# Optimization experiments

Measured on AMD Instinct MI355X. Metric: run time of the kernel, lower is better.

## Reference

```python
import math
import jax, jax.numpy as jnp
import numpy as np

HIDDEN = 1024
NUM_HEADS = 16
HEAD_DIM = HIDDEN // NUM_HEADS
B, S = 4, 2048


def setup_inputs() -> dict:
    key = jax.random.key(0)
    ks = jax.random.split(key, 10)
    sc_in = 1.0 / math.sqrt(HIDDEN)
    inp = {
        "query": jax.random.normal(ks[0], (B, S, HIDDEN), jnp.float32),
        "key": jax.random.normal(ks[1], (B, S, HIDDEN), jnp.float32),
        "value": jax.random.normal(ks[2], (B, S, HIDDEN), jnp.float32),
        "mask": jax.random.randint(ks[3], (B, S), 0, 2).astype(bool),
        # NOTE: ModuleList([Linear]*num_heads) shares ONE Linear across all heads.
        "Wq": jax.random.normal(ks[4], (HIDDEN, HEAD_DIM), jnp.float32) * sc_in,
        "bq": jnp.zeros((HEAD_DIM,), jnp.float32),
        "Wk": jax.random.normal(ks[5], (HIDDEN, HEAD_DIM), jnp.float32) * sc_in,
        "bk": jnp.zeros((HEAD_DIM,), jnp.float32),
        "Wv": jax.random.normal(ks[6], (HIDDEN, HEAD_DIM), jnp.float32) * sc_in,
        "bv": jnp.zeros((HEAD_DIM,), jnp.float32),
        "Wout": jax.random.normal(ks[7], (HIDDEN, HIDDEN), jnp.float32) * sc_in,
        "bout": jnp.zeros((HIDDEN,), jnp.float32),
        "seq_mask": 0,
    }
    return inp


def _layer_norm_scores(x, eps=1e-8):
    # torch.std is unbiased (ddof=1); is_train=False => no affine
    mean = jnp.mean(x, axis=-1, keepdims=True)
    sigma = jnp.std(x, axis=-1, keepdims=True, ddof=1)
    return (x - mean) / (sigma + eps)


def reference(query, key, value, mask, Wq, bq, Wk, bk, Wv, bv, Wout, bout, seq_mask):
    # All heads share identical weights -> compute one head, tile the concat.
    q = query @ Wq + bq          # [B,S,hd]
    k = key @ Wk + bk            # [B,S,hd]
    v = value @ Wv + bv          # [B,S,hd]
    scores = jnp.einsum("bqd,bkd->bqk", q, k) / math.sqrt(HIDDEN)  # [B,S,S]
    scores = _layer_norm_scores(scores)
    m = jnp.broadcast_to(mask[:, None, :], scores.shape)  # [B,S,S]
    if seq_mask:
        tri = jnp.triu(jnp.ones(scores.shape[-2:], bool), k=1)
        m = m | tri[None]
    # original fills with -1e-32 (effectively a no-op bug) -- reproduce exactly
    scores = scores + jnp.where(m, jnp.float32(-1e-32), jnp.float32(0.0))
    attn = jax.nn.softmax(scores, axis=-1)
    head = jnp.einsum("bqk,bkd->bqd", attn, v)   # [B,S,hd]
    attention = jnp.tile(head, (1, 1, NUM_HEADS))  # concat of identical heads
    return attention @ Wout + bout
```

## Files before the change

### kernel.cpp

```cpp
#include <hip/hip_runtime.h>
#include <math.h>

#define B_  4
#define S_  2048
#define H_  1024
#define D_  64
#define ROWS (B_*S_)
#define LOG2E 1.4426950408889634f

typedef __attribute__((ext_vector_type(4))) float  floatx4;
typedef __attribute__((ext_vector_type(8))) short  short8;
typedef __attribute__((ext_vector_type(8))) __bf16 bf16x8;

#define WS_KSUM 0
#define WS_M    (WS_KSUM + B_*D_)
#define WS_A2   (WS_M + B_*D_*D_)
#define WS_C2   (WS_A2 + ROWS)
#define WS_FEND (WS_C2 + ROWS)
#define WB_QB  0
#define WB_KF  (WB_QB + ROWS*D_)
#define WB_VF  (WB_KF + ROWS*D_)
#define WB_WT  (WB_VF + ROWS*D_)
#define WB_WFF (WB_WT + 3*D_*H_)
#define NZ2    (B_*D_ + B_*D_*D_)

__device__ __forceinline__ unsigned short f2bf(float f) {
    union { float f; unsigned u; } v; v.f = f;
    unsigned r = v.u + 0x7FFFu + ((v.u >> 16) & 1u);
    return (unsigned short)(r >> 16);
}
__device__ __forceinline__ short bfc(float f) {
    __bf16 h = (__bf16)f;
    short s; __builtin_memcpy(&s, &h, 2); return s;
}
__device__ __forceinline__ float bf2f(short s) {
    union { unsigned u; float f; } v;
    v.u = ((unsigned)(unsigned short)s) << 16; return v.f;
}
__device__ __forceinline__ bf16x8 ldb(const short* p) {
    union { short8 s; bf16x8 b; } u; u.s = *(const short8*)p; return u.b;
}
#define MFMA(a,b,c) __builtin_amdgcn_mfma_f32_16x16x32_bf16(a, b, c, 0, 0, 0)
__device__ __forceinline__ void lds_fence() {
    __builtin_amdgcn_wave_barrier();
    __builtin_amdgcn_s_waitcnt(0xc07f);
    __builtin_amdgcn_wave_barrier();
}

__global__ __launch_bounds__(256) void prep(
    const float* __restrict__ Wq, const float* __restrict__ Wk,
    const float* __restrict__ Wv, const float* __restrict__ Wout,
    float* __restrict__ wsf)
{
    __shared__ float tile[64][65];
    short* wsb = (short*)(wsf + WS_FEND);
    const int bx = blockIdx.x, t = threadIdx.x;
    if (bx < 96) {
        int idx = bx * 256 + t;
        int mat = idx >> 13, rem = idx & 8191;
        int kc = rem >> 8, nt = (rem >> 6) & 3, lane = rem & 63;
        int g = lane >> 4, l15 = lane & 15;
        const float* W = (mat == 0) ? Wq : (mat == 1) ? Wk : Wv;
        short8 fr;
        #pragma unroll
        for (int j = 0; j < 8; ++j)
            fr[j] = (short)f2bf(W[(size_t)(kc*32 + g*8 + j) * D_ + nt*16 + l15]);
        *(short8*)&wsb[WB_WT + (size_t)idx * 8] = fr;
    } else if (bx < 112) {
        int n0 = (bx - 96) * 64;
        int nn = t & 63, dg = t >> 6;
        for (int dd = 0; dd < 16; ++dd) {
            int d = dg * 16 + dd;
            float s = 0.0f;
            #pragma unroll
            for (int h = 0; h < 16; ++h)
                s += Wout[(size_t)(h * 64 + d) * H_ + n0 + nn];
            tile[d][nn] = s;
        }
        __syncthreads();
        #pragma unroll
        for (int u = 0; u < 2; ++u) {
            int s = 2*t + u;
            int ctl = s >> 7, h = (s >> 6) & 1, lane = s & 63;
            int g = lane >> 4, l2 = lane & 15;
            short8 fr;
            #pragma unroll
            for (int j = 0; j < 8; ++j)
                fr[j] = (short)f2bf(tile[h*32 + g*8 + j][ctl*16 + l2]);
            *(short8*)&wsb[WB_WFF + (size_t)((((n0 >> 4) + ctl)*2 + h)*64 + lane) * 8] = fr;
        }
    } else {
        int i = (bx - 112) * 256 + t;
        if (i < NZ2) wsf[WS_KSUM + i] = 0.0f;
    }
}

__global__ __launch_bounds__(256) void qkv_mfma(
    const float* __restrict__ query, const float* __restrict__ key,
    const float* __restrict__ value,
    const float* __restrict__ bq, const float* __restrict__ bk,
    const float* __restrict__ bvp, float* __restrict__ wsf)
{
    short* wsb = (short*)(wsf + WS_FEND);
    const int mat = blockIdx.y;
    const float* X    = (mat == 0) ? query : (mat == 1) ? key : value;
    const float* bias = (mat == 0) ? bq    : (mat == 1) ? bk  : bvp;
    const short* WT3 = wsb + WB_WT + (size_t)mat * (D_ * H_);

    const int t = threadIdx.x, w = t >> 6, lane = t & 63;
    const int l15 = lane & 15, g = lane >> 4;
    const int r0 = blockIdx.x * 32;
    const int mrow0 = (w >> 1) * 16;
    const int nt0 = (w & 1) * 2;

    __shared__ short xs[32][136];
    floatx4 acc[2] = {};

    for (int step = 0; step < 8; ++step) {
        __syncthreads();
        #pragma unroll
        for (int u = 0; u < 4; ++u) {
            int row = u * 8 + (t >> 5), col = (t & 31) * 4;
            float4 xv = *(const float4*)&X[(size_t)(r0 + row) * H_ + step * 128 + col];
            short4 pk;
            pk.x = bfc(xv.x); pk.y = bfc(xv.y); pk.z = bfc(xv.z); pk.w = bfc(xv.w);
            *(short4*)&xs[row][col] = pk;
        }
        __syncthreads();
        #pragma unroll
        for (int kk = 0; kk < 4; ++kk) {
            bf16x8 a = ldb(&xs[mrow0 + l15][kk * 32 + g * 8]);
            int kc = step * 4 + kk;
            #pragma unroll
            for (int n = 0; n < 2; ++n) {
                bf16x8 bf = ldb(&WT3[(size_t)((kc * 4) + nt0 + n) * 512 + lane * 8]);
                acc[n] = MFMA(a, bf, acc[n]);
            }
        }
    }

    if (mat == 0) {
        short* QB = wsb + WB_QB;
        #pragma unroll
        for (int n = 0; n < 2; ++n) {
            int col = (nt0 + n) * 16 + l15;
            float bb = bias[col];
            #pragma unroll
            for (int r = 0; r < 4; ++r)
                QB[(size_t)(r0 + mrow0 + 4*g + r) * D_ + col] = (short)f2bf(acc[n][r] + bb);
        }
    } else if (mat == 1) {
        short* KF = wsb + WB_KF;
        #pragma unroll
        for (int n = 0; n < 2; ++n) {
            int d = (nt0 + n) * 16 + l15;
            int kh = d >> 5, gk = (d >> 3) & 3, j = d & 7;
            float bb = bias[d];
            #pragma unroll
            for (int r = 0; r < 4; ++r) {
                int R = r0 + mrow0 + 4*g + r;
                KF[(size_t)(((R >> 4) * 2 + kh) * 64 + gk * 16 + (R & 15)) * 8 + j] =
                    (short)f2bf(acc[n][r] + bb);
            }
        }
    } else {
        short* VF = wsb + WB_VF;
        int R0 = r0 + mrow0 + 4*g;
        int kh = (R0 >> 5) & 1, gv = (R0 >> 3) & 3, j0 = R0 & 7, blk = R0 >> 6;
        #pragma unroll
        for (int n = 0; n < 2; ++n) {
            int d = (nt0 + n) * 16 + l15;
            int ntv = d >> 4;
            float bb = bias[d];
            short4 pk;
            pk.x = (short)f2bf(acc[n][0] + bb); pk.y = (short)f2bf(acc[n][1] + bb);
            pk.z = (short)f2bf(acc[n][2] + bb); pk.w = (short)f2bf(acc[n][3] + bb);
            *(short4*)&VF[(size_t)(((blk * 4 + ntv) * 2 + kh) * 64 + gv * 16 + (d & 15)) * 8 + j0] = pk;
        }
    }
}

__global__ __launch_bounds__(256) void kstats(float* __restrict__ wsf) {
    const short* KF = (short*)(wsf + WS_FEND) + WB_KF;
    const int b     = blockIdx.x >> 5;
    const int chunk = blockIdx.x & 31;
    const int keyblk0 = b * 128 + chunk * 4;

    __shared__ float kt[64][64];
    const int t = threadIdx.x;
    #pragma unroll
    for (int u = 0; u < 2; ++u) {
        int s = 2*t + u;
        int kb4 = s >> 7, kh = (s >> 6) & 1, lane2 = s & 63;
        int g2 = lane2 >> 4, l2 = lane2 & 15;
        short8 v = *(const short8*)&KF[(size_t)(((keyblk0 + kb4) * 2 + kh) * 64 + lane2) * 8];
        #pragma unroll
        for (int j = 0; j < 8; ++j)
            kt[kb4 * 16 + l2][kh * 32 + g2 * 8 + j] = bf2f(v[j]);
    }
    __syncthreads();

    const int td = t >> 4, te = t & 15;
    float acc[4][4] = {};
    for (int j = 0; j < 64; ++j) {
        float4 a  = *(const float4*)&kt[j][td*4];
        float4 bb = *(const float4*)&kt[j][te*4];
        float av[4] = {a.x, a.y, a.z, a.w};
        float bw[4] = {bb.x, bb.y, bb.z, bb.w};
        #pragma unroll
        for (int i = 0; i < 4; ++i)
            #pragma unroll
            for (int l = 0; l < 4; ++l)
                acc[i][l] += av[i] * bw[l];
    }
    float* M = wsf + WS_M + (size_t)b * D_ * D_;
    #pragma unroll
    for (int i = 0; i < 4; ++i)
        #pragma unroll
        for (int l = 0; l < 4; ++l)
            atomicAdd(&M[(td*4 + i) * D_ + te*4 + l], acc[i][l]);

    if (t < 64) {
        float s = 0.0f;
        for (int j = 0; j < 64; ++j) s += kt[j][t];
        atomicAdd(&wsf[WS_KSUM + b * D_ + t], s);
    }
}

__global__ __launch_bounds__(256) void rowstats(float* __restrict__ wsf) {
    const short* Qb = (short*)(wsf + WS_FEND) + WB_QB;
    const int t = threadIdx.x, w = t >> 6, lane = t & 63;
    const int q0 = blockIdx.x * 32 + w * 8;
    const int b  = q0 >> 11;
    const float* M = wsf + WS_M + (size_t)b * D_ * D_;

    float qv[8], y[8] = {};
    #pragma unroll
    for (int r = 0; r < 8; ++r) qv[r] = bf2f(Qb[(size_t)(q0 + r) * D_ + lane]);
    for (int d2 = 0; d2 < 64; ++d2) {
        float m = M[d2 * D_ + lane];
        #pragma unroll
        for (int r = 0; r < 8; ++r) y[r] += __shfl(qv[r], d2, 64) * m;
    }
    float kl = wsf[WS_KSUM + b * D_ + lane];
    float z[8], sv[8];
    #pragma unroll
    for (int r = 0; r < 8; ++r) { z[r] = y[r] * qv[r]; sv[r] = qv[r] * kl; }
    #pragma unroll
    for (int m = 1; m < 64; m <<= 1) {
        #pragma unroll
        for (int r = 0; r < 8; ++r) {
            z[r]  += __shfl_xor(z[r],  m, 64);
            sv[r] += __shfl_xor(sv[r], m, 64);
        }
    }
    #pragma unroll
    for (int r = 0; r < 8; ++r) {
        if (lane == r) {
            float sum   = sv[r] * (1.0f / 32.0f);
            float sumsq = z[r]  * (1.0f / 1024.0f);
            float mu  = sum * (1.0f / 2048.0f);
            float var = (sumsq - sum * sum * (1.0f / 2048.0f)) * (1.0f / 2047.0f);
            var = fmaxf(var, 0.0f);
            float inv = 1.0f / (sqrtf(var) + 1e-8f);
            wsf[WS_A2 + q0 + r] = inv * (LOG2E / 32.0f);
            wsf[WS_C2 + q0 + r] = -mu * inv * LOG2E;
        }
    }
}

__global__ __launch_bounds__(512, 4) void attn_fused(
    const float* __restrict__ bout, float* __restrict__ wsf,
    float* __restrict__ out)
{
    short* wsb = (short*)(wsf + WS_FEND);
    const short* Qb  = wsb + WB_QB;
    const short* KF  = wsb + WB_KF;
    const short* VF  = wsb + WB_VF;
    const short* WFF = wsb + WB_WFF;

    __shared__ short P[8][16][72];
    __shared__ short OL[8][16][64];
    __shared__ float sumwL[8][16];
    __shared__ short hnF[2 * 64 * 8];

    const int t = threadIdx.x, w = t >> 6, lane = t & 63;
    const int l15 = lane & 15, g = lane >> 4;
    const int q0 = blockIdx.x * 16;
    const int b  = blockIdx.x >> 7;

    bf16x8 bqf0 = ldb(&Qb[(size_t)(q0 + l15) * D_ + 0*32 + g*8]);
    bf16x8 bqf1 = ldb(&Qb[(size_t)(q0 + l15) * D_ + 1*32 + g*8]);
    const float a2v = wsf[WS_A2 + q0 + l15];
    const float c2v = wsf[WS_C2 + q0 + l15];

    floatx4 O[4] = {};
    float sacc = 0.0f;
    short* Pw = &P[w][0][0];

    for (int kc = 0; kc < 256; kc += 64) {
        const int key0 = w * 256 + kc;
        const int kblk16 = (b * S_ + key0) >> 4;
        const int kblk64 = (b * S_ + key0) >> 6;
        floatx4 Sc[4] = {};
        __builtin_amdgcn_s_setprio(1);
        #pragma unroll
        for (int kt = 0; kt < 4; ++kt) {
            bf16x8 ak0 = ldb(&KF[(size_t)(((kblk16 + kt) * 2 + 0) * 64 + lane) * 8]);
            bf16x8 ak1 = ldb(&KF[(size_t)(((kblk16 + kt) * 2 + 1) * 64 + lane) * 8]);
            Sc[kt] = MFMA(ak0, bqf0, Sc[kt]);
            Sc[kt] = MFMA(ak1, bqf1, Sc[kt]);
        }
        __builtin_amdgcn_s_setprio(0);
        lds_fence();
        #pragma unroll
        for (int kt = 0; kt < 4; ++kt) {
            float w0 = __builtin_amdgcn_exp2f(fmaf(Sc[kt][0], a2v, c2v));
            float w1 = __builtin_amdgcn_exp2f(fmaf(Sc[kt][1], a2v, c2v));
            float w2 = __builtin_amdgcn_exp2f(fmaf(Sc[kt][2], a2v, c2v));
            float w3 = __builtin_amdgcn_exp2f(fmaf(Sc[kt][3], a2v, c2v));
            sacc += (w0 + w1) + (w2 + w3);
            short4 pk;
            pk.x = bfc(w0); pk.y = bfc(w1); pk.z = bfc(w2); pk.w = bfc(w3);
            *(short4*)&Pw[l15 * 72 + kt*16 + 4*g] = pk;
        }
        lds_fence();
        bf16x8 ap0 = ldb(&Pw[l15 * 72 + 0*32 + g*8]);
        bf16x8 ap1 = ldb(&Pw[l15 * 72 + 1*32 + g*8]);
        __builtin_amdgcn_s_setprio(1);
        #pragma unroll
        for (int nt = 0; nt < 4; ++nt) {
            bf16x8 bv0 = ldb(&VF[(size_t)(((kblk64 * 4 + nt) * 2 + 0) * 64 + lane) * 8]);
            bf16x8 bv1 = ldb(&VF[(size_t)(((kblk64 * 4 + nt) * 2 + 1) * 64 + lane) * 8]);
            O[nt] = MFMA(ap0, bv0, O[nt]);
            O[nt] = MFMA(ap1, bv1, O[nt]);
        }
        __builtin_amdgcn_s_setprio(0);
    }

    sacc += __shfl_xor(sacc, 16, 64);
    sacc += __shfl_xor(sacc, 32, 64);
    if (lane < 16) sumwL[w][lane] = sacc;
    #pragma unroll
    for (int nt = 0; nt < 4; ++nt)
        #pragma unroll
        for (int r = 0; r < 4; ++r)
            OL[w][4*g + r][nt*16 + l15] = (short)f2bf(O[nt][r]);
    __syncthreads();

    {
        const int row = t >> 5;
        const int c = (t & 31) * 2;
        float s0 = 0.f, s1 = 0.f, sw = 0.f;
        #pragma unroll
        for (int p = 0; p < 8; ++p) {
            s0 += bf2f(OL[p][row][c]);
            s1 += bf2f(OL[p][row][c + 1]);
            sw += sumwL[p][row];
        }
        float inv = 1.0f / sw;
        short2 hn;
        hn.x = (short)f2bf(s0 * inv);
        hn.y = (short)f2bf(s1 * inv);
        int kh = c >> 5, g2 = (c >> 3) & 3, j = c & 7;
        *(short2*)&hnF[(kh * 64 + g2 * 16 + row) * 8 + j] = hn;
    }
    __syncthreads();

    bf16x8 ah0 = ldb(&hnF[(0 * 64 + lane) * 8]);
    bf16x8 ah1 = ldb(&hnF[(1 * 64 + lane) * 8]);
    #pragma unroll
    for (int i = 0; i < 8; ++i) {
        int n16 = w * 8 + i;
        floatx4 acc = {};
        acc = MFMA(ah0, ldb(&WFF[(size_t)(n16 * 2 + 0) * 512 + lane * 8]), acc);
        acc = MFMA(ah1, ldb(&WFF[(size_t)(n16 * 2 + 1) * 512 + lane * 8]), acc);
        int col = n16 * 16 + l15;
        float bb = bout[col];
        #pragma unroll
        for (int r = 0; r < 4; ++r)
            out[(size_t)(q0 + 4*g + r) * H_ + col] = acc[r] + bb;
    }
}

extern "C" void kernel_launch(void* const* d_in, const int* in_sizes, int n_in,
                              void* d_out, int out_size, void* d_ws, size_t ws_size,
                              hipStream_t stream) {
    const float* query = (const float*)d_in[0];
    const float* key   = (const float*)d_in[1];
    const float* value = (const float*)d_in[2];
    const float* Wq   = (const float*)d_in[4];
    const float* bq   = (const float*)d_in[5];
    const float* Wk   = (const float*)d_in[6];
    const float* bk   = (const float*)d_in[7];
    const float* Wv   = (const float*)d_in[8];
    const float* bv   = (const float*)d_in[9];
    const float* Wout = (const float*)d_in[10];
    const float* bout = (const float*)d_in[11];

    float* ws  = (float*)d_ws;
    float* out = (float*)d_out;

    prep<<<177, 256, 0, stream>>>(Wq, Wk, Wv, Wout, ws);
    qkv_mfma<<<dim3(ROWS/32, 3), 256, 0, stream>>>(query, key, value, bq, bk, bv, ws);
    kstats<<<B_ * 32, 256, 0, stream>>>(ws);
    rowstats<<<ROWS/32, 256, 0, stream>>>(ws);
    attn_fused<<<ROWS/16, 512, 0, stream>>>(bout, ws, out);
}
```

Before: 204.9 us.

## Fuse key Gram stats into QKV kernel and row stats into attention

The separate kstats kernel is removed. Its K^T K and key-sum accumulation is now done in the key-projection blocks of qkv_mfma, from the rounded bf16 values held in shared memory and added with atomics. The rowstats kernel is also removed: each attention block now computes the layernorm scale and offset for its own 16 query rows and keeps them in shared memory. This cuts two kernel launches and the round trips through the workspace. In exchange, the attention blocks do extra serial work before their main loop, and qkv gains more atomics and shared memory.

```diff
diff --git a/kernel.cpp b/kernel.cpp
--- a/kernel.cpp
+++ b/kernel.cpp
@@ -14,9 +14,7 @@
 
 #define WS_KSUM 0
 #define WS_M    (WS_KSUM + B_*D_)
-#define WS_A2   (WS_M + B_*D_*D_)
-#define WS_C2   (WS_A2 + ROWS)
-#define WS_FEND (WS_C2 + ROWS)
+#define WS_FEND (WS_M + B_*D_*D_)
 #define WB_QB  0
 #define WB_KF  (WB_QB + ROWS*D_)
 #define WB_VF  (WB_KF + ROWS*D_)
@@ -114,6 +112,7 @@
     const int nt0 = (w & 1) * 2;
 
     __shared__ short xs[32][136];
+    __shared__ float kf[32][68];
     floatx4 acc[2] = {};
 
     for (int step = 0; step < 8; ++step) {
@@ -150,7 +149,7 @@
                 QB[(size_t)(r0 + mrow0 + 4*g + r) * D_ + col] = (short)f2bf(acc[n][r] + bb);
         }
     } else if (mat == 1) {
-        short* KF = wsb + WB_KF;
+        short* KFp = wsb + WB_KF;
         #pragma unroll
         for (int n = 0; n < 2; ++n) {
             int d = (nt0 + n) * 16 + l15;
@@ -159,9 +158,38 @@
             #pragma unroll
             for (int r = 0; r < 4; ++r) {
                 int R = r0 + mrow0 + 4*g + r;
-                KF[(size_t)(((R >> 4) * 2 + kh) * 64 + gk * 16 + (R & 15)) * 8 + j] =
-                    (short)f2bf(acc[n][r] + bb);
+                unsigned short hv = f2bf(acc[n][r] + bb);
+                KFp[(size_t)(((R >> 4) * 2 + kh) * 64 + gk * 16 + (R & 15)) * 8 + j] =
+                    (short)hv;
+                kf[mrow0 + 4*g + r][d] = bf2f((short)hv);
             }
+        }
+        __syncthreads();
+        const int b = r0 >> 11;
+        const int td = t >> 4, te = t & 15;
+        float macc[4][4] = {};
+        for (int jj = 0; jj < 32; ++jj) {
+            float4 a  = *(const float4*)&kf[jj][td*4];
+            float4 bb2 = *(const float4*)&kf[jj][te*4];
+            float av[4] = {a.x, a.y, a.z, a.w};
+            float bw[4] = {bb2.x, bb2.y, bb2.z, bb2.w};
+            #pragma unroll
+            for (int i = 0; i < 4; ++i)
+                #pragma unroll
+                for (int l = 0; l < 4; ++l)
+                    macc[i][l] += av[i] * bw[l];
+        }
+        float* M = wsf + WS_M + (size_t)b * D_ * D_;
+        #pragma unroll
+        for (int i = 0; i < 4; ++i)
+            #pragma unroll
+            for (int l = 0; l < 4; ++l)
+                atomicAdd(&M[(td*4 + i) * D_ + te*4 + l], macc[i][l]);
+        if (t < 64) {
+            float s = 0.0f;
+            #pragma unroll
+            for (int jj = 0; jj < 32; ++jj) s += kf[jj][t];
+            atomicAdd(&wsf[WS_KSUM + b * D_ + t], s);
         }
     } else {
         short* VF = wsb + WB_VF;
@@ -176,95 +204,6 @@
             pk.x = (short)f2bf(acc[n][0] + bb); pk.y = (short)f2bf(acc[n][1] + bb);
             pk.z = (short)f2bf(acc[n][2] + bb); pk.w = (short)f2bf(acc[n][3] + bb);
             *(short4*)&VF[(size_t)(((blk * 4 + ntv) * 2 + kh) * 64 + gv * 16 + (d & 15)) * 8 + j0] = pk;
-        }
-    }
-}
-
-__global__ __launch_bounds__(256) void kstats(float* __restrict__ wsf) {
-    const short* KF = (short*)(wsf + WS_FEND) + WB_KF;
-    const int b     = blockIdx.x >> 5;
-    const int chunk = blockIdx.x & 31;
-    const int keyblk0 = b * 128 + chunk * 4;
-
-    __shared__ float kt[64][64];
-    const int t = threadIdx.x;
-    #pragma unroll
-    for (int u = 0; u < 2; ++u) {
-        int s = 2*t + u;
-        int kb4 = s >> 7, kh = (s >> 6) & 1, lane2 = s & 63;
-        int g2 = lane2 >> 4, l2 = lane2 & 15;
-        short8 v = *(const short8*)&KF[(size_t)(((keyblk0 + kb4) * 2 + kh) * 64 + lane2) * 8];
-        #pragma unroll
-        for (int j = 0; j < 8; ++j)
-            kt[kb4 * 16 + l2][kh * 32 + g2 * 8 + j] = bf2f(v[j]);
-    }
-    __syncthreads();
-
-    const int td = t >> 4, te = t & 15;
-    float acc[4][4] = {};
-    for (int j = 0; j < 64; ++j) {
-        float4 a  = *(const float4*)&kt[j][td*4];
-        float4 bb = *(const float4*)&kt[j][te*4];
-        float av[4] = {a.x, a.y, a.z, a.w};
-        float bw[4] = {bb.x, bb.y, bb.z, bb.w};
-        #pragma unroll
-        for (int i = 0; i < 4; ++i)
-            #pragma unroll
-            for (int l = 0; l < 4; ++l)
-                acc[i][l] += av[i] * bw[l];
-    }
-    float* M = wsf + WS_M + (size_t)b * D_ * D_;
-    #pragma unroll
-    for (int i = 0; i < 4; ++i)
-        #pragma unroll
-        for (int l = 0; l < 4; ++l)
-            atomicAdd(&M[(td*4 + i) * D_ + te*4 + l], acc[i][l]);
-
-    if (t < 64) {
-        float s = 0.0f;
-        for (int j = 0; j < 64; ++j) s += kt[j][t];
-        atomicAdd(&wsf[WS_KSUM + b * D_ + t], s);
-    }
-}
-
-__global__ __launch_bounds__(256) void rowstats(float* __restrict__ wsf) {
-    const short* Qb = (short*)(wsf + WS_FEND) + WB_QB;
-    const int t = threadIdx.x, w = t >> 6, lane = t & 63;
-    const int q0 = blockIdx.x * 32 + w * 8;
-    const int b  = q0 >> 11;
-    const float* M = wsf + WS_M + (size_t)b * D_ * D_;
-
-    float qv[8], y[8] = {};
-    #pragma unroll
-    for (int r = 0; r < 8; ++r) qv[r] = bf2f(Qb[(size_t)(q0 + r) * D_ + lane]);
-    for (int d2 = 0; d2 < 64; ++d2) {
-        float m = M[d2 * D_ + lane];
-        #pragma unroll
-        for (int r = 0; r < 8; ++r) y[r] += __shfl(qv[r], d2, 64) * m;
-    }
-    float kl = wsf[WS_KSUM + b * D_ + lane];
-    float z[8], sv[8];
-    #pragma unroll
-    for (int r = 0; r < 8; ++r) { z[r] = y[r] * qv[r]; sv[r] = qv[r] * kl; }
-    #pragma unroll
-    for (int m = 1; m < 64; m <<= 1) {
-        #pragma unroll
-        for (int r = 0; r < 8; ++r) {
-            z[r]  += __shfl_xor(z[r],  m, 64);
-            sv[r] += __shfl_xor(sv[r], m, 64);
-        }
-    }
-    #pragma unroll
-    for (int r = 0; r < 8; ++r) {
-        if (lane == r) {
-            float sum   = sv[r] * (1.0f / 32.0f);
-            float sumsq = z[r]  * (1.0f / 1024.0f);
-            float mu  = sum * (1.0f / 2048.0f);
-            float var = (sumsq - sum * sum * (1.0f / 2048.0f)) * (1.0f / 2047.0f);
-            var = fmaxf(var, 0.0f);
-            float inv = 1.0f / (sqrtf(var) + 1e-8f);
-            wsf[WS_A2 + q0 + r] = inv * (LOG2E / 32.0f);
-            wsf[WS_C2 + q0 + r] = -mu * inv * LOG2E;
         }
     }
 }
@@ -283,16 +222,56 @@
     __shared__ short OL[8][16][64];
     __shared__ float sumwL[8][16];
     __shared__ short hnF[2 * 64 * 8];
+    __shared__ float smA[16], smC[16];
 
     const int t = threadIdx.x, w = t >> 6, lane = t & 63;
     const int l15 = lane & 15, g = lane >> 4;
     const int q0 = blockIdx.x * 16;
     const int b  = blockIdx.x >> 7;
 
+    if (w < 4) {
+        const int rw = q0 + w * 4;
+        const float* M = wsf + WS_M + (size_t)b * D_ * D_;
+        float qv[4], y[4] = {};
+        #pragma unroll
+        for (int r = 0; r < 4; ++r) qv[r] = bf2f(Qb[(size_t)(rw + r) * D_ + lane]);
+        for (int d2 = 0; d2 < 64; ++d2) {
+            float m = M[d2 * D_ + lane];
+            #pragma unroll
+            for (int r = 0; r < 4; ++r) y[r] += __shfl(qv[r], d2, 64) * m;
+        }
+        float kl = wsf[WS_KSUM + b * D_ + lane];
+        float z[4], sv[4];
+        #pragma unroll
+        for (int r = 0; r < 4; ++r) { z[r] = y[r] * qv[r]; sv[r] = qv[r] * kl; }
+        #pragma unroll
+        for (int m = 1; m < 64; m <<= 1) {
+            #pragma unroll
+            for (int r = 0; r < 4; ++r) {
+                z[r]  += __shfl_xor(z[r],  m, 64);
+                sv[r] += __shfl_xor(sv[r], m, 64);
+            }
+        }
+        #pragma unroll
+        for (int r = 0; r < 4; ++r) {
+            if (lane == r) {
+                float sum   = sv[r] * (1.0f / 32.0f);
+                float sumsq = z[r]  * (1.0f / 1024.0f);
+                float mu  = sum * (1.0f / 2048.0f);
+                float var = (sumsq - sum * sum * (1.0f / 2048.0f)) * (1.0f / 2047.0f);
+                var = fmaxf(var, 0.0f);
+                float inv = 1.0f / (sqrtf(var) + 1e-8f);
+                smA[w*4 + r] = inv * (LOG2E / 32.0f);
+                smC[w*4 + r] = -mu * inv * LOG2E;
+            }
+        }
+    }
+
     bf16x8 bqf0 = ldb(&Qb[(size_t)(q0 + l15) * D_ + 0*32 + g*8]);
     bf16x8 bqf1 = ldb(&Qb[(size_t)(q0 + l15) * D_ + 1*32 + g*8]);
-    const float a2v = wsf[WS_A2 + q0 + l15];
-    const float c2v = wsf[WS_C2 + q0 + l15];
+    __syncthreads();
+    const float a2v = smA[l15];
+    const float c2v = smC[l15];
 
     floatx4 O[4] = {};
     float sacc = 0.0f;
@@ -403,7 +382,5 @@
 
     prep<<<177, 256, 0, stream>>>(Wq, Wk, Wv, Wout, ws);
     qkv_mfma<<<dim3(ROWS/32, 3), 256, 0, stream>>>(query, key, value, bq, bk, bv, ws);
-    kstats<<<B_ * 32, 256, 0, stream>>>(ws);
-    rowstats<<<ROWS/32, 256, 0, stream>>>(ws);
     attn_fused<<<ROWS/16, 512, 0, stream>>>(bout, ws, out);
 }
```

After: 199.5 us. 1.03x faster.
